# Optimization experiments

Hardware: AMD Instinct MI355X
Metric: run time of the kernel (lower is better)

## Reference

```python
import jax, jax.numpy as jnp
import numpy as np

N_NODES = 100000
N_EDGES = 1600000
N_GRAPHS = 1024
DIM_IN = 128
DIM_SELF = 16
BN_EPS = 1e-5


def _bn(x, gamma, beta):
    # training-mode BatchNorm1d over dim 0 (biased variance, as torch uses for normalization)
    m = jnp.mean(x, axis=0)
    v = jnp.mean((x - m) ** 2, axis=0)
    return gamma * (x - m) * jax.lax.rsqrt(v + BN_EPS) + beta


def _mlp(x, W1, b1, g, b, W2, b2):
    h = x @ W1 + b1
    h = jax.nn.relu(_bn(h, g, b))
    return h @ W2 + b2


def _gin(h, src, dst, W1, b1, g, b, W2, b2):
    # GINConv with eps=0: (1+eps)*h + sum over in-neighbors, then MLP
    agg = jax.ops.segment_sum(h[src], dst, num_segments=N_NODES)
    return _mlp(h + agg, W1, b1, g, b, W2, b2)


def setup_inputs() -> dict:
    key = jax.random.key(0)
    ks = jax.random.split(key, 16)

    def lin(k, fan_in, fan_out):
        bound = 1.0 / np.sqrt(fan_in)
        k1, k2 = jax.random.split(k)
        W = jax.random.uniform(k1, (fan_in, fan_out), jnp.float32, -bound, bound)
        b = jax.random.uniform(k2, (fan_out,), jnp.float32, -bound, bound)
        return W, b

    inp = {}
    inp['feat'] = jax.random.normal(ks[0], (N_NODES, DIM_IN), jnp.float32)
    inp['self_feat'] = jax.random.normal(ks[1], (N_GRAPHS, DIM_SELF), jnp.float32)
    inp['edge_src'] = jax.random.randint(ks[2], (N_EDGES,), 0, N_NODES, jnp.int32)
    inp['edge_dst'] = jax.random.randint(ks[3], (N_EDGES,), 0, N_NODES, jnp.int32)
    inp['node2graph'] = jnp.sort(jax.random.randint(ks[4], (N_NODES,), 0, N_GRAPHS, jnp.int32))

    inp['g1_W1'], inp['g1_b1'] = lin(ks[5], DIM_IN, 100)
    inp['g1_gamma'] = jnp.ones((100,), jnp.float32)
    inp['g1_beta'] = jnp.zeros((100,), jnp.float32)
    inp['g1_W2'], inp['g1_b2'] = lin(ks[6], 100, 100)

    inp['g2_W1'], inp['g2_b1'] = lin(ks[7], 100, 20)
    inp['g2_gamma'] = jnp.ones((20,), jnp.float32)
    inp['g2_beta'] = jnp.zeros((20,), jnp.float32)
    inp['g2_W2'], inp['g2_b2'] = lin(ks[8], 20, 20)

    inp['fc1_W'], inp['fc1_b'] = lin(ks[9], 20 * DIM_SELF, 32)
    inp['bn1_gamma'] = jnp.ones((32,), jnp.float32)
    inp['bn1_beta'] = jnp.zeros((32,), jnp.float32)
    inp['fc2_W'], inp['fc2_b'] = lin(ks[10], 32, 8)
    inp['bn2_gamma'] = jnp.ones((8,), jnp.float32)
    inp['bn2_beta'] = jnp.zeros((8,), jnp.float32)
    inp['fc3_W'], inp['fc3_b'] = lin(ks[11], 8, 1)
    return inp


def reference(feat, self_feat,
              g1_W1, g1_b1, g1_gamma, g1_beta, g1_W2, g1_b2,
              g2_W1, g2_b1, g2_gamma, g2_beta, g2_W2, g2_b2,
              fc1_W, fc1_b, bn1_gamma, bn1_beta,
              fc2_W, fc2_b, bn2_gamma, bn2_beta,
              fc3_W, fc3_b,
              edge_src, edge_dst, node2graph):
    h = _gin(feat, edge_src, edge_dst, g1_W1, g1_b1, g1_gamma, g1_beta, g1_W2, g1_b2)
    h = jax.nn.relu(h)
    h = _gin(h, edge_src, edge_dst, g2_W1, g2_b1, g2_gamma, g2_beta, g2_W2, g2_b2)
    h = jax.nn.relu(h)  # [N, 20]

    # dgl.mean_nodes: per-graph mean of node features
    sums = jax.ops.segment_sum(h, node2graph, num_segments=N_GRAPHS)  # [B, 20]
    cnts = jax.ops.segment_sum(jnp.ones((N_NODES,), h.dtype), node2graph, num_segments=N_GRAPHS)
    hg = sums / jnp.maximum(cnts, 1.0)[:, None]

    # kronecker fusion: bmm([B,20,1],[B,1,dim_self]) -> flatten
    kron = jnp.einsum('bi,bj->bij', hg, self_feat).reshape(N_GRAPHS, -1)  # [B, 20*dim_self]

    out = jax.nn.relu(_bn(kron @ fc1_W + fc1_b, bn1_gamma, bn1_beta))
    # dropout(0.3) is identity in eval mode
    out = jax.nn.relu(_bn(out @ fc2_W + fc2_b, bn2_gamma, bn2_beta))
    out = out @ fc3_W + fc3_b  # [B, dim_out]
    return out
```

## Files before the change

### kernel.cpp

```cpp
#include <hip/hip_runtime.h>

#define NN 100000
#define NE 1600000
#define NG 1024
#define DIN 128
#define D1 100
#define D2 20
#define DSELF 16
#define BN_EPS 1e-5f

#define NB 391
#define NBLK 782
#define EPB 2048
#define RAWCAP 5120
#define NAGG2 4000
#define NREP 64
#define APITCH 136

typedef unsigned int uint;
typedef unsigned short ushort;
typedef __attribute__((ext_vector_type(8))) short bfv8;
typedef __attribute__((ext_vector_type(4))) float fv4;

__device__ inline float bflo(uint x) { return __uint_as_float(x << 16); }
__device__ inline float bfhi(uint x) { return __uint_as_float(x & 0xffff0000u); }
__device__ inline uint packbf2(float a, float b) {
    uint ua = __float_as_uint(a), ub = __float_as_uint(b);
    ua += 0x7fffu + ((ua >> 16) & 1u);
    ub += 0x7fffu + ((ub >> 16) & 1u);
    return (ua >> 16) | (ub & 0xffff0000u);
}
__device__ inline ushort bfr(float x) {
    uint u = __float_as_uint(x);
    u += 0x7fffu + ((u >> 16) & 1u);
    return (ushort)(u >> 16);
}

__global__ __launch_bounds__(256) void k_gemm1(const float* __restrict__ feat,
                                               const float* __restrict__ W1,
                                               ushort* __restrict__ z1bf,
                                               float* __restrict__ pb1r) {
    __shared__ __align__(16) char smem[64 * APITCH * 2 + 112 * APITCH * 2];
    ushort* Al = (ushort*)smem;
    ushort* Bt = (ushort*)(smem + 64 * APITCH * 2);
    int t = threadIdx.x;
    if (blockIdx.x == 0) {
        for (int i = t; i < NREP * 200; i += 256) pb1r[i] = 0.f;
    }
    int row0 = blockIdx.x * 64;
#pragma unroll
    for (int i = 0; i < 8; i++) {
        int p = i * 256 + t;
        int r = p >> 5, cq = p & 31;
        int row = row0 + r; if (row >= NN) row = NN - 1;
        float4 v = *(const float4*)(feat + (size_t)row * DIN + cq * 4);
        ushort* dst = Al + r * APITCH + 4 * cq;
        dst[0] = bfr(v.x); dst[1] = bfr(v.y); dst[2] = bfr(v.z); dst[3] = bfr(v.w);
    }
    for (int p = t; p < 12800; p += 256) {
        int k = p / 100, n = p % 100;
        Bt[n * APITCH + k] = bfr(W1[p]);
    }
    __syncthreads();
    int w = __builtin_amdgcn_readfirstlane(t >> 6);
    int l = t & 63;
    int m16 = l & 15, quad = l >> 4;
    fv4 acc[7];
#pragma unroll
    for (int nt = 0; nt < 7; nt++) acc[nt] = (fv4){0.f, 0.f, 0.f, 0.f};
    const ushort* arow = Al + (w * 16 + m16) * APITCH;
#pragma unroll
    for (int kk = 0; kk < 4; kk++) {
        int kb = kk * 32 + quad * 8;
        bfv8 a = *(const bfv8*)(arow + kb);
#pragma unroll
        for (int nt = 0; nt < 7; nt++) {
            bfv8 b = *(const bfv8*)(Bt + (nt * 16 + m16) * APITCH + kb);
            acc[nt] = __builtin_amdgcn_mfma_f32_16x16x32_bf16(a, b, acc[nt], 0, 0, 0);
        }
    }
    __syncthreads();
    float* Ep = (float*)smem;
#pragma unroll
    for (int nt = 0; nt < 7; nt++) {
        int n = nt * 16 + m16;
        if (n < 100) {
#pragma unroll
            for (int rix = 0; rix < 4; rix++)
                Ep[(w * 16 + quad * 4 + rix) * 101 + n] = acc[nt][rix];
        }
    }
    __syncthreads();
#pragma unroll
    for (int i = 0; i < 13; i++) {
        int p = i * 256 + t;
        if (p < 3200) {
            int rr = p / 50, cc = 2 * (p % 50);
            int row = row0 + rr;
            if (row < NN) {
                float v0 = Ep[rr * 101 + cc], v1 = Ep[rr * 101 + cc + 1];
                *(uint*)(z1bf + (size_t)row * 128 + cc) = packbf2(v0, v1);
            }
        }
    }
}

__global__ __launch_bounds__(256) void k_csrA1(const int* __restrict__ dst,
                                               int* __restrict__ pbcount) {
    __shared__ int h[NB];
    int t = threadIdx.x, blk = blockIdx.x;
    for (int i = t; i < NB; i += 256) h[i] = 0;
    __syncthreads();
    int e0 = blk * EPB + t;
#pragma unroll
    for (int i = 0; i < 8; i++) {
        int e = e0 + i * 256;
        if (e < NE) atomicAdd(&h[dst[e] >> 8], 1);
    }
    __syncthreads();
    for (int i = t; i < NB; i += 256) pbcount[i * NBLK + blk] = h[i];
}

__global__ __launch_bounds__(1024) void k_csrS1(int* __restrict__ pbcount,
                                                int* __restrict__ btot) {
    __shared__ int s[1024];
    int t = threadIdx.x, b = blockIdx.x;
    int v = (t < NBLK) ? pbcount[b * NBLK + t] : 0;
    s[t] = v;
    __syncthreads();
    for (int off = 1; off < 1024; off <<= 1) {
        int x = (t >= off) ? s[t - off] : 0;
        __syncthreads();
        s[t] += x;
        __syncthreads();
    }
    if (t < NBLK) pbcount[b * NBLK + t] = s[t] - v;
    if (t == 1023) btot[b] = s[t];
}

__global__ __launch_bounds__(256) void k_csrA2(const int* __restrict__ src,
                                               const int* __restrict__ dst,
                                               const int* __restrict__ pbexcl,
                                               const int* __restrict__ btot,
                                               int* __restrict__ ebase_g,
                                               uint* __restrict__ gbuf) {
    __shared__ int cur[NB];
    __shared__ int sa[512], sb[512];
    int t = threadIdx.x, blk = blockIdx.x;
    int o0 = (t < NB) ? btot[t] : 0;
    int o1 = (t + 256 < NB) ? btot[t + 256] : 0;
    sa[t] = o0; sa[t + 256] = o1;
    __syncthreads();
    int* sp = sa; int* dp = sb;
    for (int off = 1; off < 512; off <<= 1) {
        dp[t] = sp[t] + ((t >= off) ? sp[t - off] : 0);
        int i2 = t + 256;
        dp[i2] = sp[i2] + ((i2 >= off) ? sp[i2 - off] : 0);
        __syncthreads();
        int* tmp = sp; sp = dp; dp = tmp;
    }
    if (t < NB)       cur[t]       = (sp[t] - o0) + pbexcl[t * NBLK + blk];
    if (t + 256 < NB) cur[t + 256] = (sp[t + 256] - o1) + pbexcl[(t + 256) * NBLK + blk];
    if (blk == 0) {
        if (t < NB)       ebase_g[t]       = sp[t] - o0;
        if (t + 256 < NB) ebase_g[t + 256] = sp[t + 256] - o1;
        if (t == 0)       ebase_g[NB]      = sp[NB - 1];
    }
    __syncthreads();
    int e0 = blk * EPB + t;
#pragma unroll
    for (int i = 0; i < 8; i++) {
        int e = e0 + i * 256;
        if (e < NE) {
            int d = dst[e];
            int b = d >> 8;
            int pos = atomicAdd(&cur[b], 1);
            gbuf[pos] = (uint)src[e] | ((uint)(d & 255) << 17);
        }
    }
}

__global__ __launch_bounds__(256) void k_csrB(const uint* __restrict__ gbuf,
                                              const int* __restrict__ ebase,
                                              int* __restrict__ deg,
                                              int* __restrict__ offs,
                                              int* __restrict__ srcS) {
    __shared__ uint raw[RAWCAP];
    __shared__ int srt[RAWCAP];
    __shared__ int pref[256], cur[256];
    int t = threadIdx.x, b = blockIdx.x;
    int e0 = ebase[b], e1 = ebase[b + 1];
    int cnt = e1 - e0; if (cnt > RAWCAP) cnt = RAWCAP;
    cur[t] = 0;
    for (int i = t; i < cnt; i += 256) raw[i] = gbuf[e0 + i];
    __syncthreads();
    for (int i = t; i < cnt; i += 256) atomicAdd(&cur[raw[i] >> 17], 1);
    __syncthreads();
    int v = cur[t];
    pref[t] = v;
    __syncthreads();
    for (int off = 1; off < 256; off <<= 1) {
        int x = (t >= off) ? pref[t - off] : 0;
        __syncthreads();
        pref[t] += x;
        __syncthreads();
    }
    int excl = pref[t] - v;
    int node = b * 256 + t;
    if (node < NN) { deg[node] = v; offs[node] = e0 + excl; }
    cur[t] = excl;
    __syncthreads();
    for (int i = t; i < cnt; i += 256) {
        uint p = raw[i];
        int lpos = atomicAdd(&cur[p >> 17], 1);
        srt[lpos] = (int)(p & 0x1FFFFu);
    }
    __syncthreads();
    for (int i = t; i < cnt; i += 256) srcS[e0 + i] = srt[i];
}

__global__ __launch_bounds__(256) void k_agg1(const ushort* __restrict__ z1bf,
                                              const int* __restrict__ offs,
                                              const int* __restrict__ deg,
                                              const int* __restrict__ srcS,
                                              ushort* __restrict__ u1b,
                                              float* __restrict__ pb1r,
                                              int nbase) {
    __shared__ float part[4][200];
    int t = threadIdx.x;
    int wv = __builtin_amdgcn_readfirstlane(t >> 6);
    int l = t & 63;
    bool act = l < 50;
    const ushort* zc = z1bf + 2 * l;
    float S0 = 0.f, S1 = 0.f, Q0 = 0.f, Q1 = 0.f;
    int n0 = nbase + blockIdx.x * 16 + wv * 4;
#pragma unroll 1
    for (int k = 0; k < 4; k++) {
        int n = n0 + k;
        int d = deg[n], base = offs[n];
        float a0 = 0.f, a1 = 0.f, b0 = 0.f, b1 = 0.f;
        float c0 = 0.f, c1 = 0.f, e0 = 0.f, e1 = 0.f;
        int i = 0;
        for (; i + 8 <= d; i += 8) {
            int s0 = srcS[base + i],     s1 = srcS[base + i + 1];
            int s2 = srcS[base + i + 2], s3 = srcS[base + i + 3];
            int s4 = srcS[base + i + 4], s5 = srcS[base + i + 5];
            int s6 = srcS[base + i + 6], s7 = srcS[base + i + 7];
            if (act) {
                uint x0 = *(const uint*)(zc + (size_t)s0 * 128);
                uint x1 = *(const uint*)(zc + (size_t)s1 * 128);
                uint x2 = *(const uint*)(zc + (size_t)s2 * 128);
                uint x3 = *(const uint*)(zc + (size_t)s3 * 128);
                uint x4 = *(const uint*)(zc + (size_t)s4 * 128);
                uint x5 = *(const uint*)(zc + (size_t)s5 * 128);
                uint x6 = *(const uint*)(zc + (size_t)s6 * 128);
                uint x7 = *(const uint*)(zc + (size_t)s7 * 128);
                a0 += bflo(x0); a1 += bfhi(x0);
                b0 += bflo(x1); b1 += bfhi(x1);
                c0 += bflo(x2); c1 += bfhi(x2);
                e0 += bflo(x3); e1 += bfhi(x3);
                a0 += bflo(x4); a1 += bfhi(x4);
                b0 += bflo(x5); b1 += bfhi(x5);
                c0 += bflo(x6); c1 += bfhi(x6);
                e0 += bflo(x7); e1 += bfhi(x7);
            }
        }
        for (; i + 2 <= d; i += 2) {
            int s0 = srcS[base + i], s1 = srcS[base + i + 1];
            if (act) {
                uint x0 = *(const uint*)(zc + (size_t)s0 * 128);
                uint x1 = *(const uint*)(zc + (size_t)s1 * 128);
                a0 += bflo(x0); a1 += bfhi(x0);
                b0 += bflo(x1); b1 += bfhi(x1);
            }
        }
        if (i < d) {
            int s0 = srcS[base + i];
            if (act) {
                uint x0 = *(const uint*)(zc + (size_t)s0 * 128);
                a0 += bflo(x0); a1 += bfhi(x0);
            }
        }
        if (act) {
            uint xs = *(const uint*)(zc + (size_t)n * 128);
            float r0 = (a0 + b0) + (c0 + e0) + bflo(xs);
            float r1 = (a1 + b1) + (c1 + e1) + bfhi(xs);
            *(uint*)(u1b + (size_t)n * 100 + 2 * l) = packbf2(r0, r1);
            S0 += r0; S1 += r1;
            Q0 = fmaf(r0, r0, Q0); Q1 = fmaf(r1, r1, Q1);
        }
    }
    if (act) {
        part[wv][2 * l] = S0;        part[wv][2 * l + 1] = S1;
        part[wv][100 + 2 * l] = Q0;  part[wv][100 + 2 * l + 1] = Q1;
    }
    __syncthreads();
    if (t < 200) {
        float s = part[0][t] + part[1][t] + part[2][t] + part[3][t];
        atomicAdd(&pb1r[(blockIdx.x & (NREP - 1)) * 200 + t], s);
    }
}

__global__ __launch_bounds__(256) void k_m2(const ushort* __restrict__ u1b,
                                            const float* __restrict__ pb1r,
                                            const float* __restrict__ gamma,
                                            const float* __restrict__ beta,
                                            const float* __restrict__ W2,
                                            const float* __restrict__ b2,
                                            const float* __restrict__ W1p,
                                            ushort* __restrict__ z2bf,
                                            float* __restrict__ pb2r,
                                            float* __restrict__ hgsum) {
    __shared__ float Xs[100 * 65];
    __shared__ float scW[100], shW[100];
    int t = threadIdx.x;
    if (blockIdx.x == 0) {
        for (int i = t; i < NREP * 40; i += 256) pb2r[i] = 0.f;
        for (int i = t; i < NG * D2; i += 256) hgsum[i] = 0.f;
    }
    if (t < 200) {
        float s = 0.f;
#pragma unroll 8
        for (int r = 0; r < NREP; r++) s += pb1r[r * 200 + t];
        Xs[t] = s;
    }
    __syncthreads();
    if (t < 100) {
        float S = Xs[t], Q = Xs[100 + t];
        float mean = S * (1.f / NN);
        float var = Q * (1.f / NN) - mean * mean;
        float inv = rsqrtf(var + BN_EPS);
        float s = gamma[t] * inv;
        scW[t] = s;
        shW[t] = beta[t] - mean * s;
    }
    __syncthreads();
    int row0 = blockIdx.x * 64;
#pragma unroll
    for (int i = 0; i < 13; i++) {
        int p = i * 256 + t;
        if (p < 3200) {
            int r = p / 50, c = 2 * (p % 50);
            int row = row0 + r; if (row >= NN) row = NN - 1;
            uint x = *(const uint*)(u1b + (size_t)row * 100 + c);
            Xs[c * 65 + r] = fmaxf(bflo(x) * scW[c] + shW[c], 0.f);
            Xs[(c + 1) * 65 + r] = fmaxf(bfhi(x) * scW[c + 1] + shW[c + 1], 0.f);
        }
    }
    __syncthreads();
    int cg = __builtin_amdgcn_readfirstlane(t >> 6);
    int r = t & 63;
    int j0 = cg * 25;
    float H[25];
#pragma unroll
    for (int m = 0; m < 25; m++) H[m] = 0.f;
    for (int k = 0; k < D1; k++) {
        float a = Xs[k * 65 + r];
        const float* wr = W2 + k * D1 + j0;
#pragma unroll
        for (int m = 0; m < 25; m++) H[m] = fmaf(a, wr[m], H[m]);
    }
#pragma unroll
    for (int m = 0; m < 25; m++) H[m] = fmaxf(H[m] + b2[j0 + m], 0.f);
    float pz[20];
#pragma unroll
    for (int c = 0; c < 20; c++) pz[c] = 0.f;
#pragma unroll
    for (int m = 0; m < 25; m++) {
        const float* wp = W1p + (j0 + m) * D2;
#pragma unroll
        for (int c = 0; c < 20; c++) pz[c] = fmaf(H[m], wp[c], pz[c]);
    }
    __syncthreads();
    float* red = Xs;
#pragma unroll
    for (int c = 0; c < 20; c++) red[t * 20 + c] = pz[c];
    __syncthreads();
#pragma unroll
    for (int i = 0; i < 3; i++) {
        int p = i * 256 + t;
        if (p < 640) {
            int rr = p / 10, c2 = 2 * (p % 10);
            int row = row0 + rr;
            if (row < NN) {
                float v0 = red[rr * 20 + c2] + red[(64 + rr) * 20 + c2] +
                           red[(128 + rr) * 20 + c2] + red[(192 + rr) * 20 + c2];
                float v1 = red[rr * 20 + c2 + 1] + red[(64 + rr) * 20 + c2 + 1] +
                           red[(128 + rr) * 20 + c2 + 1] + red[(192 + rr) * 20 + c2 + 1];
                *(uint*)(z2bf + (size_t)row * 32 + c2) = packbf2(v0, v1);
            }
        }
    }
}

__global__ __launch_bounds__(256) void k_agg2(const ushort* __restrict__ z2bf,
                                              const int* __restrict__ offs,
                                              const int* __restrict__ deg,
                                              const int* __restrict__ srcS,
                                              float* __restrict__ u2,
                                              float* __restrict__ pb2r) {
    __shared__ float ls[500], lq[500];
    int t = threadIdx.x;
    int n = blockIdx.x * 25 + t / 10;
    int c2 = 2 * (t % 10);
    float r0 = 0.f, r1 = 0.f;
    if (t < 250 && n < NN) {
        int d = deg[n], base = offs[n];
        const ushort* zc = z2bf + c2;
        float a0 = 0.f, a1 = 0.f, b0 = 0.f, b1 = 0.f;
        int i = 0;
        for (; i + 2 <= d; i += 2) {
            uint x0 = *(const uint*)(zc + (size_t)srcS[base + i] * 32);
            uint x1 = *(const uint*)(zc + (size_t)srcS[base + i + 1] * 32);
            a0 += bflo(x0); a1 += bfhi(x0);
            b0 += bflo(x1); b1 += bfhi(x1);
        }
        if (i < d) {
            uint x0 = *(const uint*)(zc + (size_t)srcS[base + i] * 32);
            a0 += bflo(x0); a1 += bfhi(x0);
        }
        uint xs = *(const uint*)(zc + (size_t)n * 32);
        r0 = a0 + b0 + bflo(xs);
        r1 = a1 + b1 + bfhi(xs);
        *(float2*)(u2 + (size_t)n * D2 + c2) = make_float2(r0, r1);
    }
    if (t < 250) {
        int idx = (t / 10) * 20 + c2;
        ls[idx] = r0;     lq[idx] = r0 * r0;
        ls[idx + 1] = r1; lq[idx + 1] = r1 * r1;
    }
    __syncthreads();
    if (t < 20) {
        float S = 0.f, Q = 0.f;
#pragma unroll
        for (int j = 0; j < 25; j++) { S += ls[j * 20 + t]; Q += lq[j * 20 + t]; }
        int rep = (blockIdx.x & (NREP - 1)) * 40;
        atomicAdd(&pb2r[rep + t], S);
        atomicAdd(&pb2r[rep + 20 + t], Q);
    }
}

__global__ __launch_bounds__(256) void k_m3p(const float* __restrict__ u2,
                                             const float* __restrict__ pb2r,
                                             const float* __restrict__ gamma,
                                             const float* __restrict__ beta,
                                             const float* __restrict__ W2p,
                                             const float* __restrict__ b2p,
                                             const int* __restrict__ n2g,
                                             float* __restrict__ hgsum) {
    __shared__ float X[256][21];
    __shared__ int gl[256];
    __shared__ float red40[40], scB[20], shB[20];
    int t = threadIdx.x;
    if (t < 40) {
        float s = 0.f;
#pragma unroll 8
        for (int r = 0; r < NREP; r++) s += pb2r[r * 40 + t];
        red40[t] = s;
    }
    __syncthreads();
    if (t < 20) {
        float S = red40[t], Q = red40[20 + t];
        float mean = S * (1.f / NN);
        float var = Q * (1.f / NN) - mean * mean;
        float inv = rsqrtf(var + BN_EPS);
        float s = gamma[t] * inv;
        scB[t] = s;
        shB[t] = beta[t] - mean * s;
    }
    __syncthreads();
    int row = blockIdx.x * 256 + t;
    bool valid = row < NN;
    gl[t] = valid ? n2g[row] : -1;
    if (valid) {
        float ya[20];
        const float4* up = (const float4*)(u2 + (size_t)row * D2);
#pragma unroll
        for (int i = 0; i < 5; i++) {
            float4 v = up[i];
            ya[4 * i + 0] = fmaxf(v.x * scB[4 * i + 0] + shB[4 * i + 0], 0.f);
            ya[4 * i + 1] = fmaxf(v.y * scB[4 * i + 1] + shB[4 * i + 1], 0.f);
            ya[4 * i + 2] = fmaxf(v.z * scB[4 * i + 2] + shB[4 * i + 2], 0.f);
            ya[4 * i + 3] = fmaxf(v.w * scB[4 * i + 3] + shB[4 * i + 3], 0.f);
        }
#pragma unroll
        for (int j = 0; j < D2; j++) {
            float h = b2p[j];
#pragma unroll
            for (int k = 0; k < D2; k++) h = fmaf(ya[k], W2p[k * D2 + j], h);
            X[t][j] = fmaxf(h, 0.f);
        }
    } else {
#pragma unroll
        for (int j = 0; j < D2; j++) X[t][j] = 0.f;
    }
    __syncthreads();
    if (t < 160) {
        int seg = t / 20, j = t % 20;
        int i0 = seg * 32, i1 = i0 + 32;
        int gprev = -2;
        float acc = 0.f;
        for (int i = i0; i < i1; i++) {
            int gi = gl[i];
            if (gi != gprev) {
                if (gprev >= 0) atomicAdd(&hgsum[gprev * D2 + j], acc);
                gprev = gi; acc = 0.f;
            }
            acc += X[i][j];
        }
        if (gprev >= 0) atomicAdd(&hgsum[gprev * D2 + j], acc);
    }
}

__global__ void k_head1(const float* __restrict__ hgsum, const int* __restrict__ n2g,
                        const float* __restrict__ sf,
                        const float* __restrict__ fc1W, float* __restrict__ a1) {
    int b = blockIdx.x * 8 + threadIdx.x / 32;
    int c = threadIdx.x % 32;
    if (b >= NG) return;
    int lo = 0, hi2 = NN;
    while (lo < hi2) { int mid = (lo + hi2) >> 1; if (n2g[mid] < b) lo = mid + 1; else hi2 = mid; }
    int s0 = lo;
    hi2 = NN;
    while (lo < hi2) { int mid = (lo + hi2) >> 1; if (n2g[mid] < b + 1) lo = mid + 1; else hi2 = mid; }
    float rc = 1.f / fmaxf((float)(lo - s0), 1.f);
    const float* hgb = hgsum + b * D2;
    const float* sfb = sf + b * DSELF;
    float acc = 0.f;
    for (int i = 0; i < D2; i++) {
        float hv = hgb[i] * rc;
#pragma unroll
        for (int j = 0; j < DSELF; j++)
            acc += hv * sfb[j] * fc1W[(i * DSELF + j) * 32 + c];
    }
    a1[b * 32 + c] = acc;
}

__global__ __launch_bounds__(1024) void k_head2(
    const float* __restrict__ a1, const float* __restrict__ g1,
    const float* __restrict__ be1, const float* __restrict__ fc2W,
    const float* __restrict__ g2, const float* __restrict__ be2,
    const float* __restrict__ fc3W, const float* __restrict__ fc3b,
    float* __restrict__ out) {
    int t = threadIdx.x;
    int lane = t & 63, w = t >> 6;
    __shared__ float s1[16][32], s2[16][32];
    __shared__ float sc[32], sh[32], sc2[8], sh2[8];
    float x[32];
    const float4* ap = (const float4*)(a1 + t * 32);
#pragma unroll
    for (int i = 0; i < 8; i++) {
        float4 v = ap[i];
        x[4 * i] = v.x; x[4 * i + 1] = v.y; x[4 * i + 2] = v.z; x[4 * i + 3] = v.w;
    }
#pragma unroll
    for (int c = 0; c < 32; c++) {
        float v = x[c], q = v * v;
        for (int o = 32; o > 0; o >>= 1) {
            v += __shfl_down(v, o, 64);
            q += __shfl_down(q, o, 64);
        }
        if (lane == 0) { s1[w][c] = v; s2[w][c] = q; }
    }
    __syncthreads();
    if (t < 32) {
        float s = 0.f, q = 0.f;
        for (int ww = 0; ww < 16; ww++) { s += s1[ww][t]; q += s2[ww][t]; }
        float mean = s * (1.f / NG);
        float var = q * (1.f / NG) - mean * mean;
        float inv = rsqrtf(var + BN_EPS);
        float scl = g1[t] * inv;
        sc[t] = scl;
        sh[t] = be1[t] - mean * scl;
    }
    __syncthreads();
#pragma unroll
    for (int c = 0; c < 32; c++) x[c] = fmaxf(x[c] * sc[c] + sh[c], 0.f);
    float y[8];
#pragma unroll
    for (int p = 0; p < 8; p++) {
        float a = 0.f;
#pragma unroll
        for (int c = 0; c < 32; c++) a += x[c] * fc2W[c * 8 + p];
        y[p] = a;
    }
    __syncthreads();
#pragma unroll
    for (int p = 0; p < 8; p++) {
        float v = y[p], q = v * v;
        for (int o = 32; o > 0; o >>= 1) {
            v += __shfl_down(v, o, 64);
            q += __shfl_down(q, o, 64);
        }
        if (lane == 0) { s1[w][p] = v; s2[w][p] = q; }
    }
    __syncthreads();
    if (t < 8) {
        float s = 0.f, q = 0.f;
        for (int ww = 0; ww < 16; ww++) { s += s1[ww][t]; q += s2[ww][t]; }
        float mean = s * (1.f / NG);
        float var = q * (1.f / NG) - mean * mean;
        float inv = rsqrtf(var + BN_EPS);
        float scl = g2[t] * inv;
        sc2[t] = scl;
        sh2[t] = be2[t] - mean * scl;
    }
    __syncthreads();
    float o = fc3b[0];
#pragma unroll
    for (int p = 0; p < 8; p++) {
        float yy = fmaxf(y[p] * sc2[p] + sh2[p], 0.f);
        o += yy * fc3W[p];
    }
    out[t] = o;
}

extern "C" void kernel_launch(void* const* d_in, const int* in_sizes, int n_in,
                              void* d_out, int out_size, void* d_ws, size_t ws_size,
                              hipStream_t stream) {
    const float* feat    = (const float*)d_in[0];
    const float* sf      = (const float*)d_in[1];
    const int*   esrc    = (const int*)d_in[2];
    const int*   edst    = (const int*)d_in[3];
    const int*   n2g     = (const int*)d_in[4];
    const float* g1W1    = (const float*)d_in[5];
    const float* g1gam   = (const float*)d_in[7];
    const float* g1bet   = (const float*)d_in[8];
    const float* g1W2    = (const float*)d_in[9];
    const float* g1b2    = (const float*)d_in[10];
    const float* g2W1    = (const float*)d_in[11];
    const float* g2gam   = (const float*)d_in[13];
    const float* g2bet   = (const float*)d_in[14];
    const float* g2W2    = (const float*)d_in[15];
    const float* g2b2    = (const float*)d_in[16];
    const float* fc1W    = (const float*)d_in[17];
    const float* hbn1g   = (const float*)d_in[19];
    const float* hbn1b   = (const float*)d_in[20];
    const float* fc2W    = (const float*)d_in[21];
    const float* hbn2g   = (const float*)d_in[23];
    const float* hbn2b   = (const float*)d_in[24];
    const float* fc3W    = (const float*)d_in[25];
    const float* fc3b    = (const float*)d_in[26];
    float* out = (float*)d_out;

    char* w = (char*)d_ws;
    size_t off = 0;
    auto alloc = [&](size_t bytes) -> char* {
        char* p = w + off;
        off += (bytes + 15) & ~(size_t)15;
        return p;
    };
    char* regA = alloc((size_t)NN * 128 * 2);
    ushort* z1bf = (ushort*)regA;
    ushort* z2bf = (ushort*)regA;
    float*  u2   = (float*)(regA + 6400000);
    ushort* u1b  = (ushort*)alloc((size_t)NN * 100 * 2);
    int*   pbcnt = (int*)alloc((size_t)NB * NBLK * 4);
    int*   btot  = (int*)alloc(NB * 4);
    int*   ebase = (int*)alloc((NB + 1) * 4);
    uint*  gbuf  = (uint*)alloc((size_t)NE * 4);
    int*   deg   = (int*)alloc(NN * 4);
    int*   offs  = (int*)alloc(NN * 4);
    int*   srcS  = (int*)alloc((size_t)NE * 4);
    float* pb1r  = (float*)alloc((size_t)NREP * 200 * 4);
    float* pb2r  = (float*)alloc((size_t)NREP * 40 * 4);
    float* hgsum = (float*)alloc((size_t)NG * D2 * 4);
    float* a1    = (float*)alloc(NG * 32 * 4);
    (void)in_sizes; (void)n_in; (void)out_size; (void)ws_size;

    k_gemm1<<<(NN + 63) / 64, 256, 0, stream>>>(feat, g1W1, z1bf, pb1r);

    k_csrA1<<<NBLK, 256, 0, stream>>>(edst, pbcnt);
    k_csrS1<<<NB, 1024, 0, stream>>>(pbcnt, btot);
    k_csrA2<<<NBLK, 256, 0, stream>>>(esrc, edst, pbcnt, btot, ebase, gbuf);
    k_csrB<<<NB, 256, 0, stream>>>(gbuf, ebase, deg, offs, srcS);

    k_agg1<<<2084, 256, 0, stream>>>(z1bf, offs, deg, srcS, u1b, pb1r, 0);
    k_agg1<<<2084, 256, 0, stream>>>(z1bf, offs, deg, srcS, u1b, pb1r, 33344);
    k_agg1<<<2082, 256, 0, stream>>>(z1bf, offs, deg, srcS, u1b, pb1r, 66688);

    k_m2<<<(NN + 63) / 64, 256, 0, stream>>>(u1b, pb1r, g1gam, g1bet, g1W2, g1b2, g2W1,
                                             z2bf, pb2r, hgsum);

    k_agg2<<<NAGG2, 256, 0, stream>>>(z2bf, offs, deg, srcS, u2, pb2r);
    k_m3p<<<(NN + 255) / 256, 256, 0, stream>>>(u2, pb2r, g2gam, g2bet, g2W2, g2b2, n2g, hgsum);

    k_head1<<<NG / 8, 256, 0, stream>>>(hgsum, n2g, sf, fc1W, a1);
    k_head2<<<1, 1024, 0, stream>>>(a1, hbn1g, hbn1b, fc2W, hbn2g, hbn2b, fc3W, fc3b, out);
}
```

Baseline: 428.9 us.

## Use split-bf16 MFMA for k_m2 GEMMs and merge agg1 launches

Rewrites the two small dense GEMMs in k_m2 (100x100 then 100x20) to use bf16 MFMA 16x16x32 instructions. Precision is kept by splitting each value into high and low bf16 parts and issuing three MFMAs per tile. Weight fragments are pre-split and packed into MFMA layout by the first 9 blocks of k_csrA1, and activations are staged as hi/lo bf16 in padded shared memory. The three k_agg1 launches are also merged into a single launch. In exchange it adds rounding error compared with fp32 FMA and extra weight-prep work in the CSR kernel.

```diff
diff --git a/kernel.cpp b/kernel.cpp
--- a/kernel.cpp
+++ b/kernel.cpp
@@ -24,6 +24,7 @@
 
 __device__ inline float bflo(uint x) { return __uint_as_float(x << 16); }
 __device__ inline float bfhi(uint x) { return __uint_as_float(x & 0xffff0000u); }
+__device__ inline float bfval(ushort h) { return __uint_as_float(((uint)h) << 16); }
 __device__ inline uint packbf2(float a, float b) {
     uint ua = __float_as_uint(a), ub = __float_as_uint(b);
     ua += 0x7fffu + ((ua >> 16) & 1u);
@@ -106,9 +107,38 @@
 }
 
 __global__ __launch_bounds__(256) void k_csrA1(const int* __restrict__ dst,
-                                               int* __restrict__ pbcount) {
+                                               int* __restrict__ pbcount,
+                                               const float* __restrict__ W2,
+                                               const float* __restrict__ W1p,
+                                               ushort* __restrict__ W2fh,
+                                               ushort* __restrict__ W2fl,
+                                               ushort* __restrict__ W1pfh,
+                                               ushort* __restrict__ W1pfl) {
     __shared__ int h[NB];
     int t = threadIdx.x, blk = blockIdx.x;
+    if (blk < 9) {
+#pragma unroll
+        for (int i2 = 0; i2 < 8; i2++) {
+            int idx = blk * 2048 + i2 * 256 + t;
+            int l = (idx >> 3) & 63, j = idx & 7;
+            int kq = (l >> 4) * 8 + j;
+            int n16 = l & 15;
+            if (idx < 14336) {
+                int tile = idx >> 9; int nt = tile >> 2, kk = tile & 3;
+                int k = kk * 32 + kq, n = nt * 16 + n16;
+                float v = (k < 100 && n < 100) ? W2[k * 100 + n] : 0.f;
+                ushort hh = bfr(v);
+                W2fh[idx] = hh; W2fl[idx] = bfr(v - bfval(hh));
+            } else {
+                int idx2 = idx - 14336;
+                int tile = idx2 >> 9; int nt = tile >> 2, kk = tile & 3;
+                int k = kk * 32 + kq, n = nt * 16 + n16;
+                float v = (k < 100 && n < 20) ? W1p[k * 20 + n] : 0.f;
+                ushort hh = bfr(v);
+                W1pfh[idx2] = hh; W1pfl[idx2] = bfr(v - bfval(hh));
+            }
+        }
+    }
     for (int i = t; i < NB; i += 256) h[i] = 0;
     __syncthreads();
     int e0 = blk * EPB + t;
@@ -224,8 +254,7 @@
                                               const int* __restrict__ deg,
                                               const int* __restrict__ srcS,
                                               ushort* __restrict__ u1b,
-                                              float* __restrict__ pb1r,
-                                              int nbase) {
+                                              float* __restrict__ pb1r) {
     __shared__ float part[4][200];
     int t = threadIdx.x;
     int wv = __builtin_amdgcn_readfirstlane(t >> 6);
@@ -233,7 +262,7 @@
     bool act = l < 50;
     const ushort* zc = z1bf + 2 * l;
     float S0 = 0.f, S1 = 0.f, Q0 = 0.f, Q1 = 0.f;
-    int n0 = nbase + blockIdx.x * 16 + wv * 4;
+    int n0 = blockIdx.x * 16 + wv * 4;
 #pragma unroll 1
     for (int k = 0; k < 4; k++) {
         int n = n0 + k;
@@ -305,13 +334,17 @@
                                             const float* __restrict__ pb1r,
                                             const float* __restrict__ gamma,
                                             const float* __restrict__ beta,
-                                            const float* __restrict__ W2,
+                                            const ushort* __restrict__ W2fh,
+                                            const ushort* __restrict__ W2fl,
                                             const float* __restrict__ b2,
-                                            const float* __restrict__ W1p,
+                                            const ushort* __restrict__ W1pfh,
+                                            const ushort* __restrict__ W1pfl,
                                             ushort* __restrict__ z2bf,
                                             float* __restrict__ pb2r,
                                             float* __restrict__ hgsum) {
-    __shared__ float Xs[100 * 65];
+    __shared__ __align__(16) ushort Ah[64 * APITCH];
+    __shared__ __align__(16) ushort Alo[64 * APITCH];
+    __shared__ float red200[200];
     __shared__ float scW[100], shW[100];
     int t = threadIdx.x;
     if (blockIdx.x == 0) {
@@ -322,11 +355,16 @@
         float s = 0.f;
 #pragma unroll 8
         for (int r = 0; r < NREP; r++) s += pb1r[r * 200 + t];
-        Xs[t] = s;
+        red200[t] = s;
+    }
+    for (int p = t; p < 896; p += 256) {
+        int r = p / 14, c = 100 + 2 * (p % 14);
+        *(uint*)(Ah + r * APITCH + c) = 0u;
+        *(uint*)(Alo + r * APITCH + c) = 0u;
     }
     __syncthreads();
     if (t < 100) {
-        float S = Xs[t], Q = Xs[100 + t];
+        float S = red200[t], Q = red200[100 + t];
         float mean = S * (1.f / NN);
         float var = Q * (1.f / NN) - mean * mean;
         float inv = rsqrtf(var + BN_EPS);
@@ -343,51 +381,85 @@
             int r = p / 50, c = 2 * (p % 50);
             int row = row0 + r; if (row >= NN) row = NN - 1;
             uint x = *(const uint*)(u1b + (size_t)row * 100 + c);
-            Xs[c * 65 + r] = fmaxf(bflo(x) * scW[c] + shW[c], 0.f);
-            Xs[(c + 1) * 65 + r] = fmaxf(bfhi(x) * scW[c + 1] + shW[c + 1], 0.f);
-        }
-    }
-    __syncthreads();
-    int cg = __builtin_amdgcn_readfirstlane(t >> 6);
-    int r = t & 63;
-    int j0 = cg * 25;
-    float H[25];
-#pragma unroll
-    for (int m = 0; m < 25; m++) H[m] = 0.f;
-    for (int k = 0; k < D1; k++) {
-        float a = Xs[k * 65 + r];
-        const float* wr = W2 + k * D1 + j0;
-#pragma unroll
-        for (int m = 0; m < 25; m++) H[m] = fmaf(a, wr[m], H[m]);
-    }
-#pragma unroll
-    for (int m = 0; m < 25; m++) H[m] = fmaxf(H[m] + b2[j0 + m], 0.f);
-    float pz[20];
-#pragma unroll
-    for (int c = 0; c < 20; c++) pz[c] = 0.f;
-#pragma unroll
-    for (int m = 0; m < 25; m++) {
-        const float* wp = W1p + (j0 + m) * D2;
-#pragma unroll
-        for (int c = 0; c < 20; c++) pz[c] = fmaf(H[m], wp[c], pz[c]);
-    }
-    __syncthreads();
-    float* red = Xs;
-#pragma unroll
-    for (int c = 0; c < 20; c++) red[t * 20 + c] = pz[c];
-    __syncthreads();
-#pragma unroll
-    for (int i = 0; i < 3; i++) {
-        int p = i * 256 + t;
-        if (p < 640) {
-            int rr = p / 10, c2 = 2 * (p % 10);
-            int row = row0 + rr;
-            if (row < NN) {
-                float v0 = red[rr * 20 + c2] + red[(64 + rr) * 20 + c2] +
-                           red[(128 + rr) * 20 + c2] + red[(192 + rr) * 20 + c2];
-                float v1 = red[rr * 20 + c2 + 1] + red[(64 + rr) * 20 + c2 + 1] +
-                           red[(128 + rr) * 20 + c2 + 1] + red[(192 + rr) * 20 + c2 + 1];
-                *(uint*)(z2bf + (size_t)row * 32 + c2) = packbf2(v0, v1);
+            float y0 = fmaxf(bflo(x) * scW[c] + shW[c], 0.f);
+            float y1 = fmaxf(bfhi(x) * scW[c + 1] + shW[c + 1], 0.f);
+            ushort h0 = bfr(y0), h1 = bfr(y1);
+            ushort l0 = bfr(y0 - bfval(h0)), l1 = bfr(y1 - bfval(h1));
+            *(uint*)(Ah + r * APITCH + c) = (uint)h0 | ((uint)h1 << 16);
+            *(uint*)(Alo + r * APITCH + c) = (uint)l0 | ((uint)l1 << 16);
+        }
+    }
+    __syncthreads();
+    int w = __builtin_amdgcn_readfirstlane(t >> 6);
+    int l = t & 63;
+    int m16 = l & 15, quad = l >> 4;
+    fv4 acc[7];
+#pragma unroll
+    for (int nt = 0; nt < 7; nt++) acc[nt] = (fv4){0.f, 0.f, 0.f, 0.f};
+    {
+        const ushort* arH = Ah + (w * 16 + m16) * APITCH;
+        const ushort* arL = Alo + (w * 16 + m16) * APITCH;
+#pragma unroll
+        for (int kk = 0; kk < 4; kk++) {
+            int kb = kk * 32 + quad * 8;
+            bfv8 ah = *(const bfv8*)(arH + kb);
+            bfv8 al = *(const bfv8*)(arL + kb);
+#pragma unroll
+            for (int nt = 0; nt < 7; nt++) {
+                int fo = ((nt * 4 + kk) << 9) + l * 8;
+                bfv8 bh = *(const bfv8*)(W2fh + fo);
+                bfv8 bl = *(const bfv8*)(W2fl + fo);
+                acc[nt] = __builtin_amdgcn_mfma_f32_16x16x32_bf16(ah, bh, acc[nt], 0, 0, 0);
+                acc[nt] = __builtin_amdgcn_mfma_f32_16x16x32_bf16(ah, bl, acc[nt], 0, 0, 0);
+                acc[nt] = __builtin_amdgcn_mfma_f32_16x16x32_bf16(al, bh, acc[nt], 0, 0, 0);
+            }
+        }
+    }
+    __syncthreads();
+#pragma unroll
+    for (int nt = 0; nt < 7; nt++) {
+        int n = nt * 16 + m16;
+        float bb = (n < 100) ? b2[n] : 0.f;
+#pragma unroll
+        for (int rix = 0; rix < 4; rix++) {
+            int r = w * 16 + quad * 4 + rix;
+            float hv = (n < 100) ? fmaxf(acc[nt][rix] + bb, 0.f) : 0.f;
+            ushort hh = bfr(hv);
+            Ah[r * APITCH + n] = hh;
+            Alo[r * APITCH + n] = bfr(hv - bfval(hh));
+        }
+    }
+    __syncthreads();
+    fv4 acc2[2];
+    acc2[0] = (fv4){0.f, 0.f, 0.f, 0.f};
+    acc2[1] = (fv4){0.f, 0.f, 0.f, 0.f};
+    {
+        const ushort* arH = Ah + (w * 16 + m16) * APITCH;
+        const ushort* arL = Alo + (w * 16 + m16) * APITCH;
+#pragma unroll
+        for (int kk = 0; kk < 4; kk++) {
+            int kb = kk * 32 + quad * 8;
+            bfv8 ah = *(const bfv8*)(arH + kb);
+            bfv8 al = *(const bfv8*)(arL + kb);
+#pragma unroll
+            for (int nt = 0; nt < 2; nt++) {
+                int fo = ((nt * 4 + kk) << 9) + l * 8;
+                bfv8 bh = *(const bfv8*)(W1pfh + fo);
+                bfv8 bl = *(const bfv8*)(W1pfl + fo);
+                acc2[nt] = __builtin_amdgcn_mfma_f32_16x16x32_bf16(ah, bh, acc2[nt], 0, 0, 0);
+                acc2[nt] = __builtin_amdgcn_mfma_f32_16x16x32_bf16(ah, bl, acc2[nt], 0, 0, 0);
+                acc2[nt] = __builtin_amdgcn_mfma_f32_16x16x32_bf16(al, bh, acc2[nt], 0, 0, 0);
+            }
+        }
+    }
+#pragma unroll
+    for (int nt = 0; nt < 2; nt++) {
+        int c = nt * 16 + m16;
+        if (c < 20) {
+#pragma unroll
+            for (int rix = 0; rix < 4; rix++) {
+                int row = row0 + w * 16 + quad * 4 + rix;
+                if (row < NN) z2bf[(size_t)row * 32 + c] = bfr(acc2[nt][rix]);
             }
         }
     }
@@ -664,23 +736,25 @@
     int*   srcS  = (int*)alloc((size_t)NE * 4);
     float* pb1r  = (float*)alloc((size_t)NREP * 200 * 4);
     float* pb2r  = (float*)alloc((size_t)NREP * 40 * 4);
+    ushort* W2fh = (ushort*)alloc(14336 * 2);
+    ushort* W2fl = (ushort*)alloc(14336 * 2);
+    ushort* W1pfh = (ushort*)alloc(4096 * 2);
+    ushort* W1pfl = (ushort*)alloc(4096 * 2);
     float* hgsum = (float*)alloc((size_t)NG * D2 * 4);
     float* a1    = (float*)alloc(NG * 32 * 4);
     (void)in_sizes; (void)n_in; (void)out_size; (void)ws_size;
 
     k_gemm1<<<(NN + 63) / 64, 256, 0, stream>>>(feat, g1W1, z1bf, pb1r);
 
-    k_csrA1<<<NBLK, 256, 0, stream>>>(edst, pbcnt);
+    k_csrA1<<<NBLK, 256, 0, stream>>>(edst, pbcnt, g1W2, g2W1, W2fh, W2fl, W1pfh, W1pfl);
     k_csrS1<<<NB, 1024, 0, stream>>>(pbcnt, btot);
     k_csrA2<<<NBLK, 256, 0, stream>>>(esrc, edst, pbcnt, btot, ebase, gbuf);
     k_csrB<<<NB, 256, 0, stream>>>(gbuf, ebase, deg, offs, srcS);
 
-    k_agg1<<<2084, 256, 0, stream>>>(z1bf, offs, deg, srcS, u1b, pb1r, 0);
-    k_agg1<<<2084, 256, 0, stream>>>(z1bf, offs, deg, srcS, u1b, pb1r, 33344);
-    k_agg1<<<2082, 256, 0, stream>>>(z1bf, offs, deg, srcS, u1b, pb1r, 66688);
-
-    k_m2<<<(NN + 63) / 64, 256, 0, stream>>>(u1b, pb1r, g1gam, g1bet, g1W2, g1b2, g2W1,
-                                             z2bf, pb2r, hgsum);
+    k_agg1<<<NN / 16, 256, 0, stream>>>(z1bf, offs, deg, srcS, u1b, pb1r);
+
+    k_m2<<<(NN + 63) / 64, 256, 0, stream>>>(u1b, pb1r, g1gam, g1bet, W2fh, W2fl, g1b2,
+                                             W1pfh, W1pfl, z2bf, pb2r, hgsum);
 
     k_agg2<<<NAGG2, 256, 0, stream>>>(z2bf, offs, deg, srcS, u2, pb2r);
     k_m3p<<<(NN + 255) / 256, 256, 0, stream>>>(u2, pb2r, g2gam, g2bet, g2W2, g2b2, n2g, hgsum);
```

After: 394.7 us. 1.09x faster.
